# Optimization experiments

Measured on AMD Instinct MI355X. Metric: run time of the kernel, lower is better.

Reference implementation:

```python
import jax, jax.numpy as jnp
import numpy as np

N, IN, HID, HEADS, OUT, E = 50000, 128, 64, 4, 128, 800000
NEG_SLOPE = 0.2


def _gat_conv(x, src, dst, W, a_src, a_dst, b, heads, ch, concat):
    # x: [N, F_in]; W: [F_in, heads*ch]; a_src/a_dst: [heads, ch]; b: [heads*ch] or [ch]
    n = x.shape[0]
    h = (x @ W).reshape(n, heads, ch)                       # [N,H,C]
    al_s = jnp.einsum('nhc,hc->nh', h, a_src)               # [N,H]
    al_d = jnp.einsum('nhc,hc->nh', h, a_dst)               # [N,H]
    e = jax.nn.leaky_relu(al_s[src] + al_d[dst], NEG_SLOPE)  # [E,H]
    # segment softmax over destination nodes (every node has a self-loop)
    m = jax.ops.segment_max(e, dst, num_segments=n)
    ex = jnp.exp(e - m[dst])
    denom = jax.ops.segment_sum(ex, dst, num_segments=n)
    alpha = ex / denom[dst]                                  # [E,H]
    msg = h[src] * alpha[:, :, None]                         # [E,H,C]
    out = jax.ops.segment_sum(msg, dst, num_segments=n)      # [N,H,C]
    out = out.reshape(n, heads * ch) if concat else out.mean(axis=1)
    return out + b


def setup_inputs() -> dict:
    key = jax.random.key(0)
    ks = jax.random.split(key, 10)
    s = 0.1
    return {
        'node_features': jax.random.normal(ks[0], (N, IN), jnp.float32),
        'edge_index': jax.random.randint(ks[1], (2, E), 0, N, jnp.int64),
        'W1': jax.random.normal(ks[2], (IN, HEADS * HID), jnp.float32) * s,
        'a1_src': jax.random.normal(ks[3], (HEADS, HID), jnp.float32) * s,
        'a1_dst': jax.random.normal(ks[4], (HEADS, HID), jnp.float32) * s,
        'b1': jnp.zeros((HEADS * HID,), jnp.float32),
        'W2': jax.random.normal(ks[5], (HEADS * HID, OUT), jnp.float32) * s,
        'a2_src': jax.random.normal(ks[6], (1, OUT), jnp.float32) * s,
        'a2_dst': jax.random.normal(ks[7], (1, OUT), jnp.float32) * s,
        'b2': jnp.zeros((OUT,), jnp.float32),
    }


def reference(node_features, edge_index, W1, a1_src, a1_dst, b1, W2, a2_src, a2_dst, b2):
    n = node_features.shape[0]
    loops = jnp.arange(n, dtype=edge_index.dtype)
    src = jnp.concatenate([edge_index[0], loops])  # PyG adds self-loops by default
    dst = jnp.concatenate([edge_index[1], loops])
    x = _gat_conv(node_features, src, dst, W1, a1_src, a1_dst, b1, HEADS, HID, True)
    x = jax.nn.relu(x)
    x = _gat_conv(x, src, dst, W2, a2_src, a2_dst, b2, 1, OUT, False)
    return x
```

## Files before the change

kernel.cpp:

```cpp
#include <hip/hip_runtime.h>
#include <math.h>

#define N_NODES 50000
#define F_IN    128
#define HIDC    64
#define HEADS   4
#define C1      (HEADS*HIDC)
#define F_OUT   128
#define NE      800000
#define NET     (NE + N_NODES)
#define NEG_SLOPE 0.2f

#define NPB   49
#define NBUCK 1021
#define BPAD  16
#define K4CAP 2048

typedef unsigned short ushort_t;
typedef signed char    schar_t;
typedef __attribute__((ext_vector_type(8))) short bf16x8;
typedef __attribute__((ext_vector_type(8))) unsigned short us8;
typedef __attribute__((ext_vector_type(4))) float f32x4;

__device__ __forceinline__ float b2f(ushort_t x) {
  return __uint_as_float(((unsigned int)x) << 16);
}
__device__ __forceinline__ ushort_t f2bf(float f) {
  unsigned int u = __float_as_uint(f);
  return (ushort_t)((u + 0x7fffu + ((u >> 16) & 1u)) >> 16);
}
__device__ __forceinline__ float u2f_lo(unsigned int u) { return __uint_as_float(u << 16); }
__device__ __forceinline__ float u2f_hi(unsigned int u) { return __uint_as_float(u & 0xffff0000u); }

__device__ __forceinline__ void fma8v(float ww, uint4 vv, float* a) {
  a[0] = fmaf(ww, u2f_lo(vv.x), a[0]); a[1] = fmaf(ww, u2f_hi(vv.x), a[1]);
  a[2] = fmaf(ww, u2f_lo(vv.y), a[2]); a[3] = fmaf(ww, u2f_hi(vv.y), a[3]);
  a[4] = fmaf(ww, u2f_lo(vv.z), a[4]); a[5] = fmaf(ww, u2f_hi(vv.z), a[5]);
  a[6] = fmaf(ww, u2f_lo(vv.w), a[6]); a[7] = fmaf(ww, u2f_hi(vv.w), a[7]);
}
__device__ __forceinline__ void fma8q(float wsc, uint2 vv, float* a) {
  int x = (int)vv.x, y = (int)vv.y;
  a[0] = fmaf(wsc, (float)(schar_t)(x),        a[0]);
  a[1] = fmaf(wsc, (float)(schar_t)(x >> 8),   a[1]);
  a[2] = fmaf(wsc, (float)(schar_t)(x >> 16),  a[2]);
  a[3] = fmaf(wsc, (float)(x >> 24),           a[3]);
  a[4] = fmaf(wsc, (float)(schar_t)(y),        a[4]);
  a[5] = fmaf(wsc, (float)(schar_t)(y >> 8),   a[5]);
  a[6] = fmaf(wsc, (float)(schar_t)(y >> 16),  a[6]);
  a[7] = fmaf(wsc, (float)(y >> 24),           a[7]);
}


__global__ __launch_bounds__(256) void bucket_count(const int* __restrict__ ei,
                                                    int* __restrict__ bcnt) {
  __shared__ int hist[NBUCK];
  for (int i = threadIdx.x; i < NBUCK; i += 256) hist[i] = 0;
  __syncthreads();
  int stride = gridDim.x * 256;
  for (int e = blockIdx.x * 256 + threadIdx.x; e < NET; e += stride) {
    int d = (e < NE) ? ei[NE + e] : (e - NE);
    atomicAdd(&hist[d / NPB], 1);
  }
  __syncthreads();
  for (int i = threadIdx.x; i < NBUCK; i += 256)
    if (hist[i]) atomicAdd(&bcnt[i * BPAD], hist[i]);
}

__global__ __launch_bounds__(1024) void scan_buckets(const int* __restrict__ bcnt,
                                                     int* __restrict__ boff) {
  __shared__ int sh[1024];
  int t = threadIdx.x;
  sh[t] = (t < NBUCK) ? bcnt[t * BPAD] : 0;
  __syncthreads();
#pragma unroll
  for (int off = 1; off < 1024; off <<= 1) {
    int u = (t >= off) ? sh[t - off] : 0;
    __syncthreads();
    sh[t] += u;
    __syncthreads();
  }
  if (t < NBUCK) boff[t + 1] = sh[t];
  if (t == 0) boff[0] = 0;
}

__global__ void bucket_scatter(const int* __restrict__ ei, const int* __restrict__ boff,
                               int* __restrict__ bfill, int2* __restrict__ pairs) {
  int e = blockIdx.x * blockDim.x + threadIdx.x;
  if (e >= NET) return;
  int s, d;
  if (e < NE) { s = ei[e]; d = ei[NE + e]; }
  else        { s = e - NE; d = s; }
  int b = d / NPB;
  int pos = atomicAdd(&bfill[b * BPAD], 1);
  pairs[boff[b] + pos] = make_int2(s, d);
}

__global__ __launch_bounds__(256) void build_csr(const int2* __restrict__ pairs,
                                                 const int* __restrict__ boff,
                                                 int* __restrict__ rowptr,
                                                 int* __restrict__ colsrc) {
  __shared__ int cnt[NPB];
  __shared__ int loc[NPB + 1];
  __shared__ int2 buf[K4CAP];
  int b = blockIdx.x, t = threadIdx.x;
  int p0 = boff[b], p1 = boff[b + 1];
  int m = p1 - p0;
  int n0 = b * NPB;
  int nn = min(NPB, N_NODES - n0);
  for (int i = t; i < NPB; i += 256) cnt[i] = 0;
  __syncthreads();
  bool inlds = (m <= K4CAP);
  for (int i = t; i < m; i += 256) {
    int2 p = pairs[p0 + i];
    if (inlds) buf[i] = p;
    atomicAdd(&cnt[p.y - n0], 1);
  }
  __syncthreads();
  if (t == 0) {
    int run = 0;
#pragma unroll 1
    for (int j = 0; j < nn; ++j) { loc[j] = run; run += cnt[j]; }
    loc[nn] = run;
  }
  __syncthreads();
  for (int j = t; j < nn; j += 256) rowptr[n0 + j] = p0 + loc[j];
  if (t == 0 && n0 + nn == N_NODES) rowptr[N_NODES] = NET;
  for (int i = t; i < NPB; i += 256) cnt[i] = 0;
  __syncthreads();
  for (int i = t; i < m; i += 256) {
    int2 p = inlds ? buf[i] : pairs[p0 + i];
    int j = p.y - n0;
    int pos = atomicAdd(&cnt[j], 1);
    colsrc[p0 + loc[j] + pos] = p.x;
  }
}


__global__ void transpose_both(const float* __restrict__ W1, ushort_t* __restrict__ W1t,
                               const float* __restrict__ W2, ushort_t* __restrict__ W2t) {
  int idx = blockIdx.x * blockDim.x + threadIdx.x;
  if (idx < F_IN * C1) {
    int k = idx / C1, n = idx - k * C1;
    W1t[(size_t)n * F_IN + k] = f2bf(W1[idx]);
  } else {
    int j = idx - F_IN * C1;
    if (j < C1 * F_OUT) {
      int k = j / F_OUT, n = j - k * F_OUT;
      W2t[(size_t)n * C1 + k] = f2bf(W2[j]);
    }
  }
}


#define BKS 64
#define LDT 72

__device__ __forceinline__ us8 stage8(const ushort_t* p) { return *(const us8*)p; }
__device__ __forceinline__ us8 stage8(const float* p) {
  float4 f0 = *(const float4*)p;
  float4 f1 = *(const float4*)(p + 4);
  us8 o;
  o[0] = f2bf(f0.x); o[1] = f2bf(f0.y); o[2] = f2bf(f0.z); o[3] = f2bf(f0.w);
  o[4] = f2bf(f1.x); o[5] = f2bf(f1.y); o[6] = f2bf(f1.z); o[7] = f2bf(f1.w);
  return o;
}

template<int K, int NCOL, int AL_MODE, typename AT, typename CT>
__global__ __launch_bounds__(256) void gemm_mfma(const AT* __restrict__ A,
                                                 const ushort_t* __restrict__ Bt,
                                                 CT* __restrict__ C,
                                                 float* __restrict__ scales,
                                                 const float* __restrict__ a_s,
                                                 const float* __restrict__ a_d,
                                                 float* __restrict__ als,
                                                 float* __restrict__ ald) {
  __shared__ __align__(16) char smem[2 * 128 * LDT * 2];
  ushort_t (*Asl)[LDT] = (ushort_t(*)[LDT])smem;
  ushort_t (*Bsl)[LDT] = (ushort_t(*)[LDT])(smem + 128 * LDT * 2);

  const int tid = threadIdx.x;
  const int lane = tid & 63;
  const int wave = tid >> 6;
  const int wr = wave >> 1, wc = wave & 1;
  const int row0 = blockIdx.y * 128;
  const int col0 = blockIdx.x * 128;
  const int l15 = lane & 15, l4 = lane >> 4;

  f32x4 acc[4][4] = {};

  for (int k0 = 0; k0 < K; k0 += BKS) {
#pragma unroll
    for (int i = 0; i < 4; ++i) {
      int seg = tid + i * 256;
      int row = seg >> 3, kq = (seg & 7) * 8;
      int arow = row0 + row;
      us8 v = {0, 0, 0, 0, 0, 0, 0, 0};
      if (arow < N_NODES) v = stage8(&A[(size_t)arow * K + k0 + kq]);
      *(us8*)&Asl[row][kq] = v;
    }
#pragma unroll
    for (int i = 0; i < 4; ++i) {
      int seg = tid + i * 256;
      int row = seg >> 3, kq = (seg & 7) * 8;
      us8 v = *(const us8*)&Bt[(size_t)(col0 + row) * K + k0 + kq];
      *(us8*)&Bsl[row][kq] = v;
    }
    __syncthreads();
#pragma unroll
    for (int kk = 0; kk < BKS; kk += 32) {
      bf16x8 af[4], bfr[4];
#pragma unroll
      for (int mi = 0; mi < 4; ++mi)
        af[mi] = *(const bf16x8*)&Asl[wr * 64 + mi * 16 + l15][kk + l4 * 8];
#pragma unroll
      for (int ni = 0; ni < 4; ++ni)
        bfr[ni] = *(const bf16x8*)&Bsl[wc * 64 + ni * 16 + l15][kk + l4 * 8];
#pragma unroll
      for (int mi = 0; mi < 4; ++mi)
#pragma unroll
        for (int ni = 0; ni < 4; ++ni)
          acc[mi][ni] = __builtin_amdgcn_mfma_f32_16x16x32_bf16(af[mi], bfr[ni], acc[mi][ni], 0, 0, 0);
    }
    __syncthreads();
  }

  {
    const int albase = (AL_MODE == 1 ? col0 : 0) + wc * 64;
    float asv[4], adv[4];
#pragma unroll
    for (int ni = 0; ni < 4; ++ni) {
      asv[ni] = a_s[albase + ni * 16 + l15];
      adv[ni] = a_d[albase + ni * 16 + l15];
    }
#pragma unroll
    for (int mi = 0; mi < 4; ++mi) {
      float ps[4], pd[4];
#pragma unroll
      for (int r = 0; r < 4; ++r) {
        ps[r] = acc[mi][0][r] * asv[0] + acc[mi][1][r] * asv[1] +
                acc[mi][2][r] * asv[2] + acc[mi][3][r] * asv[3];
        pd[r] = acc[mi][0][r] * adv[0] + acc[mi][1][r] * adv[1] +
                acc[mi][2][r] * adv[2] + acc[mi][3][r] * adv[3];
      }
#pragma unroll
      for (int m = 1; m < 16; m <<= 1) {
#pragma unroll
        for (int r = 0; r < 4; ++r) {
          ps[r] += __shfl_xor(ps[r], m, 64);
          pd[r] += __shfl_xor(pd[r], m, 64);
        }
      }
      if (l15 == 0) {
#pragma unroll
        for (int r = 0; r < 4; ++r) {
          int row = row0 + wr * 64 + mi * 16 + l4 * 4 + r;
          if (row < N_NODES) {
            if (AL_MODE == 1) {
              int h = albase >> 6;
              als[row * 4 + h] = ps[r];
              ald[row * 4 + h] = pd[r];
            } else {
              atomicAdd(&als[row], ps[r]);
              atomicAdd(&ald[row], pd[r]);
            }
          }
        }
      }
    }
  }

  {
    ushort_t (*Ep)[136] = (ushort_t(*)[136])smem;
#pragma unroll
    for (int mi = 0; mi < 4; ++mi)
#pragma unroll
      for (int ni = 0; ni < 4; ++ni)
#pragma unroll
        for (int r = 0; r < 4; ++r)
          Ep[wr * 64 + mi * 16 + l4 * 4 + r][wc * 64 + ni * 16 + l15] = f2bf(acc[mi][ni][r]);
    __syncthreads();
    int row = tid >> 1, half = tid & 1;
    int grow = row0 + row;
    if (grow < N_NODES) {
      if constexpr (sizeof(CT) == 1) {
        float vals[64];
        float amax = 0.f;
#pragma unroll
        for (int i = 0; i < 8; ++i) {
          us8 v = *(const us8*)&Ep[row][half * 64 + i * 8];
#pragma unroll
          for (int j = 0; j < 8; ++j) {
            float f = b2f((ushort_t)v[j]);
            vals[i * 8 + j] = f;
            amax = fmaxf(amax, fabsf(f));
          }
        }
        float inv = amax > 0.f ? 127.f / amax : 0.f;
        scales[grow * 4 + (col0 >> 6) + half] = amax * (1.f / 127.f);
        schar_t ob[64];
#pragma unroll
        for (int i = 0; i < 64; ++i)
          ob[i] = (schar_t)(int)rintf(vals[i] * inv);
#pragma unroll
        for (int i = 0; i < 4; ++i)
          *(us8*)&C[(size_t)grow * NCOL + col0 + half * 64 + i * 16] =
              *(const us8*)&ob[i * 16];
      } else {
#pragma unroll
        for (int i = 0; i < 8; ++i)
          *(us8*)&C[(size_t)grow * NCOL + col0 + half * 64 + i * 8] =
              *(const us8*)&Ep[row][half * 64 + i * 8];
      }
    }
  }
}


__global__ __launch_bounds__(256) void agg1(const int* __restrict__ rowptr,
                                            const int* __restrict__ colsrc,
                                            const schar_t* __restrict__ Hq,
                                            const float* __restrict__ Sc,
                                            const float* __restrict__ als,
                                            const float* __restrict__ ald,
                                            const float* __restrict__ b1,
                                            ushort_t* __restrict__ X2b) {
  int wave = threadIdx.x >> 6, lane = threadIdx.x & 63;
  int n = blockIdx.x * 4 + wave;
  if (n >= N_NODES) return;
  int half = lane >> 5, li = lane & 31, h = li >> 3;
  float ad = ald[n * 4 + h];
  int beg = rowptr[n], end = rowptr[n + 1];
  float a[8] = {};
  float s = 0.f;
  int i = beg + half;
  for (; i + 6 < end; i += 8) {
    int s0 = colsrc[i], s1 = colsrc[i + 2], s2 = colsrc[i + 4], s3 = colsrc[i + 6];
    float sc0 = als[s0 * 4 + h] + ad;
    float sc1 = als[s1 * 4 + h] + ad;
    float sc2 = als[s2 * 4 + h] + ad;
    float sc3 = als[s3 * 4 + h] + ad;
    float q0 = Sc[s0 * 4 + h], q1 = Sc[s1 * 4 + h], q2 = Sc[s2 * 4 + h], q3 = Sc[s3 * 4 + h];
    uint2 v0 = *(const uint2*)&Hq[(size_t)s0 * C1 + li * 8];
    uint2 v1 = *(const uint2*)&Hq[(size_t)s1 * C1 + li * 8];
    uint2 v2 = *(const uint2*)&Hq[(size_t)s2 * C1 + li * 8];
    uint2 v3 = *(const uint2*)&Hq[(size_t)s3 * C1 + li * 8];
    sc0 = sc0 > 0.f ? sc0 : NEG_SLOPE * sc0;
    sc1 = sc1 > 0.f ? sc1 : NEG_SLOPE * sc1;
    sc2 = sc2 > 0.f ? sc2 : NEG_SLOPE * sc2;
    sc3 = sc3 > 0.f ? sc3 : NEG_SLOPE * sc3;
    float w0 = __expf(sc0), w1 = __expf(sc1), w2 = __expf(sc2), w3 = __expf(sc3);
    s += (w0 + w1) + (w2 + w3);
    fma8q(w0 * q0, v0, a); fma8q(w1 * q1, v1, a);
    fma8q(w2 * q2, v2, a); fma8q(w3 * q3, v3, a);
  }
  for (; i + 2 < end; i += 4) {
    int s0 = colsrc[i], s1 = colsrc[i + 2];
    float sc0 = als[s0 * 4 + h] + ad;
    float sc1 = als[s1 * 4 + h] + ad;
    float q0 = Sc[s0 * 4 + h], q1 = Sc[s1 * 4 + h];
    uint2 v0 = *(const uint2*)&Hq[(size_t)s0 * C1 + li * 8];
    uint2 v1 = *(const uint2*)&Hq[(size_t)s1 * C1 + li * 8];
    sc0 = sc0 > 0.f ? sc0 : NEG_SLOPE * sc0;
    sc1 = sc1 > 0.f ? sc1 : NEG_SLOPE * sc1;
    float w0 = __expf(sc0), w1 = __expf(sc1);
    s += w0 + w1;
    fma8q(w0 * q0, v0, a); fma8q(w1 * q1, v1, a);
  }
  for (; i < end; i += 2) {
    int s0 = colsrc[i];
    float sc0 = als[s0 * 4 + h] + ad;
    float q0 = Sc[s0 * 4 + h];
    uint2 v0 = *(const uint2*)&Hq[(size_t)s0 * C1 + li * 8];
    sc0 = sc0 > 0.f ? sc0 : NEG_SLOPE * sc0;
    float w0 = __expf(sc0);
    s += w0;
    fma8q(w0 * q0, v0, a);
  }
#pragma unroll
  for (int j = 0; j < 8; ++j) a[j] += __shfl_xor(a[j], 32, 64);
  s += __shfl_xor(s, 32, 64);
  if (lane < 32) {
    float si = 1.f / s;
    int c = li * 8;
    float4 bb0 = *(const float4*)&b1[c];
    float4 bb1 = *(const float4*)&b1[c + 4];
    ushort_t o[8];
    o[0] = f2bf(fmaxf(a[0] * si + bb0.x, 0.f));
    o[1] = f2bf(fmaxf(a[1] * si + bb0.y, 0.f));
    o[2] = f2bf(fmaxf(a[2] * si + bb0.z, 0.f));
    o[3] = f2bf(fmaxf(a[3] * si + bb0.w, 0.f));
    o[4] = f2bf(fmaxf(a[4] * si + bb1.x, 0.f));
    o[5] = f2bf(fmaxf(a[5] * si + bb1.y, 0.f));
    o[6] = f2bf(fmaxf(a[6] * si + bb1.z, 0.f));
    o[7] = f2bf(fmaxf(a[7] * si + bb1.w, 0.f));
    *(us8*)&X2b[(size_t)n * C1 + c] = *(const us8*)o;
  }
}

__global__ __launch_bounds__(256) void agg2(const int* __restrict__ rowptr,
                                            const int* __restrict__ colsrc,
                                            const ushort_t* __restrict__ Hb,
                                            const float* __restrict__ als,
                                            const float* __restrict__ ald,
                                            const float* __restrict__ b2,
                                            float* __restrict__ out) {
  int wave = threadIdx.x >> 6, lane = threadIdx.x & 63;
  int n = blockIdx.x * 4 + wave;
  if (n >= N_NODES) return;
  int quarter = lane >> 4, li = lane & 15;
  float ad = ald[n];
  int beg = rowptr[n], end = rowptr[n + 1];
  float a[8] = {};
  float s = 0.f;
  int i = beg + quarter;
  for (; i + 12 < end; i += 16) {
    int s0 = colsrc[i], s1 = colsrc[i + 4], s2 = colsrc[i + 8], s3 = colsrc[i + 12];
    float sc0 = als[s0] + ad;
    float sc1 = als[s1] + ad;
    float sc2 = als[s2] + ad;
    float sc3 = als[s3] + ad;
    uint4 v0 = *(const uint4*)&Hb[(size_t)s0 * F_OUT + li * 8];
    uint4 v1 = *(const uint4*)&Hb[(size_t)s1 * F_OUT + li * 8];
    uint4 v2 = *(const uint4*)&Hb[(size_t)s2 * F_OUT + li * 8];
    uint4 v3 = *(const uint4*)&Hb[(size_t)s3 * F_OUT + li * 8];
    sc0 = sc0 > 0.f ? sc0 : NEG_SLOPE * sc0;
    sc1 = sc1 > 0.f ? sc1 : NEG_SLOPE * sc1;
    sc2 = sc2 > 0.f ? sc2 : NEG_SLOPE * sc2;
    sc3 = sc3 > 0.f ? sc3 : NEG_SLOPE * sc3;
    float w0 = __expf(sc0), w1 = __expf(sc1), w2 = __expf(sc2), w3 = __expf(sc3);
    s += (w0 + w1) + (w2 + w3);
    fma8v(w0, v0, a); fma8v(w1, v1, a); fma8v(w2, v2, a); fma8v(w3, v3, a);
  }
  for (; i + 4 < end; i += 8) {
    int s0 = colsrc[i], s1 = colsrc[i + 4];
    float sc0 = als[s0] + ad;
    float sc1 = als[s1] + ad;
    uint4 v0 = *(const uint4*)&Hb[(size_t)s0 * F_OUT + li * 8];
    uint4 v1 = *(const uint4*)&Hb[(size_t)s1 * F_OUT + li * 8];
    sc0 = sc0 > 0.f ? sc0 : NEG_SLOPE * sc0;
    sc1 = sc1 > 0.f ? sc1 : NEG_SLOPE * sc1;
    float w0 = __expf(sc0), w1 = __expf(sc1);
    s += w0 + w1;
    fma8v(w0, v0, a); fma8v(w1, v1, a);
  }
  for (; i < end; i += 4) {
    int s0 = colsrc[i];
    float sc0 = als[s0] + ad;
    uint4 v0 = *(const uint4*)&Hb[(size_t)s0 * F_OUT + li * 8];
    sc0 = sc0 > 0.f ? sc0 : NEG_SLOPE * sc0;
    float w0 = __expf(sc0);
    s += w0;
    fma8v(w0, v0, a);
  }
#pragma unroll
  for (int j = 0; j < 8; ++j) a[j] += __shfl_xor(a[j], 16, 64);
#pragma unroll
  for (int j = 0; j < 8; ++j) a[j] += __shfl_xor(a[j], 32, 64);
  s += __shfl_xor(s, 16, 64);
  s += __shfl_xor(s, 32, 64);
  if (lane < 16) {
    float si = 1.f / s;
    int c = li * 8;
    float4 bb0 = *(const float4*)&b2[c];
    float4 bb1 = *(const float4*)&b2[c + 4];
    float4 o0, o1;
    o0.x = a[0] * si + bb0.x; o0.y = a[1] * si + bb0.y;
    o0.z = a[2] * si + bb0.z; o0.w = a[3] * si + bb0.w;
    o1.x = a[4] * si + bb1.x; o1.y = a[5] * si + bb1.y;
    o1.z = a[6] * si + bb1.z; o1.w = a[7] * si + bb1.w;
    *(float4*)&out[(size_t)n * F_OUT + c] = o0;
    *(float4*)&out[(size_t)n * F_OUT + c + 4] = o1;
  }
}


extern "C" void kernel_launch(void* const* d_in, const int* in_sizes, int n_in,
                              void* d_out, int out_size, void* d_ws, size_t ws_size,
                              hipStream_t stream) {
  const float* X   = (const float*)d_in[0];
  const int*   EI  = (const int*)d_in[1];
  const float* W1  = (const float*)d_in[2];
  const float* a1s = (const float*)d_in[3];
  const float* a1d = (const float*)d_in[4];
  const float* b1  = (const float*)d_in[5];
  const float* W2  = (const float*)d_in[6];
  const float* a2s = (const float*)d_in[7];
  const float* a2d = (const float*)d_in[8];
  const float* b2  = (const float*)d_in[9];
  float* out = (float*)d_out;

  char* ws = (char*)d_ws;
  size_t off = 0;
  auto alloc = [&](size_t bytes) -> void* {
    void* p = ws + off;
    off += (bytes + 255) & ~(size_t)255;
    return p;
  };
  int* bcnt       = (int*)alloc((size_t)NBUCK * BPAD * 4);
  int* bfill      = (int*)alloc((size_t)NBUCK * BPAD * 4);
  float* ALS2     = (float*)alloc((size_t)N_NODES * 4);
  float* ALD2     = (float*)alloc((size_t)N_NODES * 4);
  size_t zero_span = off;
  int* boff       = (int*)alloc((size_t)(NBUCK + 1) * 4);
  int* rowptr     = (int*)alloc((size_t)(N_NODES + 1) * 4);
  int* colsrc     = (int*)alloc((size_t)NET * 4);
  int2* pairs     = (int2*)alloc((size_t)NET * 8);
  ushort_t* W1t   = (ushort_t*)alloc((size_t)C1 * F_IN * 2);
  ushort_t* W2t   = (ushort_t*)alloc((size_t)F_OUT * C1 * 2);
  schar_t* H1q    = (schar_t*)alloc((size_t)N_NODES * C1);
  float* SC1      = (float*)alloc((size_t)N_NODES * HEADS * 4);
  float* ALS1     = (float*)alloc((size_t)N_NODES * HEADS * 4);
  float* ALD1     = (float*)alloc((size_t)N_NODES * HEADS * 4);
  ushort_t* X2b   = (ushort_t*)alloc((size_t)N_NODES * C1 * 2);
  ushort_t* H2b = (ushort_t*)H1q;

  hipMemsetAsync(ws, 0, zero_span, stream);

  bucket_count<<<128, 256, 0, stream>>>(EI, bcnt);
  scan_buckets<<<1, 1024, 0, stream>>>(bcnt, boff);
  bucket_scatter<<<(NET + 255) / 256, 256, 0, stream>>>(EI, boff, bfill, pairs);
  build_csr<<<NBUCK, 256, 0, stream>>>(pairs, boff, rowptr, colsrc);

  transpose_both<<<(F_IN * C1 + C1 * F_OUT + 255) / 256, 256, 0, stream>>>(W1, W1t, W2, W2t);

  {
    dim3 grid(C1 / 128, (N_NODES + 127) / 128);
    gemm_mfma<F_IN, C1, 1, float, schar_t><<<grid, 256, 0, stream>>>(
        X, W1t, H1q, SC1, a1s, a1d, ALS1, ALD1);
  }
  agg1<<<(N_NODES + 3) / 4, 256, 0, stream>>>(rowptr, colsrc, H1q, SC1, ALS1, ALD1, b1, X2b);

  {
    dim3 grid(F_OUT / 128, (N_NODES + 127) / 128);
    gemm_mfma<C1, F_OUT, 2, ushort_t, ushort_t><<<grid, 256, 0, stream>>>(
        X2b, W2t, H2b, nullptr, a2s, a2d, ALS2, ALD2);
  }
  agg2<<<(N_NODES + 3) / 4, 256, 0, stream>>>(rowptr, colsrc, H2b, ALS2, ALD2, b2, out);
}
```

Before: 207.2 us.

## Aggregate bucket scatter atomics per block via shared-memory histogram

Replaces the per-edge global atomicAdd in bucket scatter with a blocked version. Each 1024-thread block builds a local histogram of destination buckets for its 8192-edge chunk in LDS, reserves a contiguous range per bucket with one global atomic, then scatters using LDS atomics. This cuts global atomic contention on the 1021 bucket counters. In exchange the edge indices are read twice and the grid has only about 104 blocks.

```diff
diff --git a/kernel.cpp b/kernel.cpp
--- a/kernel.cpp
+++ b/kernel.cpp
@@ -15,6 +15,7 @@
 #define NBUCK 1021
 #define BPAD  16
 #define K4CAP 2048
+#define SCHUNK 8192
 
 typedef unsigned short ushort_t;
 typedef signed char    schar_t;
@@ -83,16 +84,33 @@
   if (t == 0) boff[0] = 0;
 }
 
-__global__ void bucket_scatter(const int* __restrict__ ei, const int* __restrict__ boff,
-                               int* __restrict__ bfill, int2* __restrict__ pairs) {
-  int e = blockIdx.x * blockDim.x + threadIdx.x;
-  if (e >= NET) return;
-  int s, d;
-  if (e < NE) { s = ei[e]; d = ei[NE + e]; }
-  else        { s = e - NE; d = s; }
-  int b = d / NPB;
-  int pos = atomicAdd(&bfill[b * BPAD], 1);
-  pairs[boff[b] + pos] = make_int2(s, d);
+__global__ __launch_bounds__(1024) void bucket_scatter_blocked(const int* __restrict__ ei,
+                                                               const int* __restrict__ boff,
+                                                               int* __restrict__ bfill,
+                                                               int2* __restrict__ pairs) {
+  __shared__ int hist[NBUCK];
+  __shared__ int gbase[NBUCK];
+  __shared__ int fill[NBUCK];
+  int c0 = blockIdx.x * SCHUNK;
+  int cend = min(c0 + SCHUNK, NET);
+  for (int i = threadIdx.x; i < NBUCK; i += 1024) { hist[i] = 0; fill[i] = 0; }
+  __syncthreads();
+  for (int e = c0 + threadIdx.x; e < cend; e += 1024) {
+    int d = (e < NE) ? ei[NE + e] : (e - NE);
+    atomicAdd(&hist[d / NPB], 1);
+  }
+  __syncthreads();
+  for (int i = threadIdx.x; i < NBUCK; i += 1024)
+    if (hist[i]) gbase[i] = boff[i] + atomicAdd(&bfill[i * BPAD], hist[i]);
+  __syncthreads();
+  for (int e = c0 + threadIdx.x; e < cend; e += 1024) {
+    int s, d;
+    if (e < NE) { s = ei[e]; d = ei[NE + e]; }
+    else        { s = e - NE; d = s; }
+    int b = d / NPB;
+    int lpos = atomicAdd(&fill[b], 1);
+    pairs[gbase[b] + lpos] = make_int2(s, d);
+  }
 }
 
 __global__ __launch_bounds__(256) void build_csr(const int2* __restrict__ pairs,
@@ -518,7 +536,7 @@
 
   bucket_count<<<128, 256, 0, stream>>>(EI, bcnt);
   scan_buckets<<<1, 1024, 0, stream>>>(bcnt, boff);
-  bucket_scatter<<<(NET + 255) / 256, 256, 0, stream>>>(EI, boff, bfill, pairs);
+  bucket_scatter_blocked<<<(NET + SCHUNK - 1) / SCHUNK, 1024, 0, stream>>>(EI, boff, bfill, pairs);
   build_csr<<<NBUCK, 256, 0, stream>>>(pairs, boff, rowptr, colsrc);
 
   transpose_both<<<(F_IN * C1 + C1 * F_OUT + 255) / 256, 256, 0, stream>>>(W1, W1t, W2, W2t);
```

After: 176.0 us. 1.18x faster.
